# Kernel optimization log

Hardware: AMD Instinct MI355X
Metric: run time of the kernel (lower is better)

## Reference

```python
import jax, jax.numpy as jnp
import numpy as np

N, D, H, O, E, K = 4096, 512, 1024, 512, 8, 2


def setup_inputs() -> dict:
    key = jax.random.key(0)
    ks = jax.random.split(key, 7)
    s = 0.02
    return {
        "x": jax.random.normal(ks[0], (N, D), dtype=jnp.float32),
        "W1": jax.random.normal(ks[1], (E, D, H), dtype=jnp.float32) * s,
        "b1": jnp.zeros((E, H), dtype=jnp.float32),
        "W2": jax.random.normal(ks[2], (E, H, O), dtype=jnp.float32) * s,
        "b2": jnp.zeros((E, O), dtype=jnp.float32),
        "Wg": jax.random.normal(ks[3], (D, E), dtype=jnp.float32) * s,
        "bg": jnp.zeros((E,), dtype=jnp.float32),
        "k": K,
    }


def reference(x, W1, b1, W2, b2, Wg, bg, k):
    # Gating: softmax over experts, then top-k with renormalized weights
    gates = jax.nn.softmax(x @ Wg + bg, axis=1)              # [N, E]
    topv, topi = jax.lax.top_k(gates, k)                     # [N, k]
    w = topv / jnp.sum(topv, axis=1, keepdims=True)          # renormalized top-k weights

    # Dense per-expert two-layer MLP (grouped GEMM form)
    h = jax.nn.relu(jnp.einsum('nd,edh->neh', x, W1) + b1[None])   # [N, E, H]
    y = jnp.einsum('neh,eho->neo', h, W2) + b2[None]               # [N, E, O]

    # Gather selected experts and combine
    y_sel = jnp.take_along_axis(y, topi[:, :, None], axis=1)       # [N, k, O]
    out = jnp.einsum('nko,nk->no', y_sel, w)                       # [N, O]
    return out, gates, topi
```

## Files before the change

kernel.cpp:

```cpp
#include <hip/hip_runtime.h>
#include <hip/hip_bf16.h>

#define N_TOK 4096
#define DIM   512
#define HID   1024
#define OUTD  512
#define NEXP  8
#define TOPK  2

#define MT1 72
#define HROWS 9216

typedef __bf16 bf16;
typedef bf16  bf16x8 __attribute__((ext_vector_type(8)));
typedef bf16  bf16x4 __attribute__((ext_vector_type(4)));
typedef float f32x4  __attribute__((ext_vector_type(4)));

__device__ inline f32x4 mfma16(bf16x8 a, bf16x8 b, f32x4 c) {
    return __builtin_amdgcn_mfma_f32_16x16x32_bf16(a, b, c, 0, 0, 0);
}

__device__ inline void gload16(const bf16* g, char* l) {
    __builtin_amdgcn_global_load_lds(
        (const __attribute__((address_space(1))) void*)g,
        (__attribute__((address_space(3))) void*)l, 16, 0, 0);
}

__global__ __launch_bounds__(256) void prep_kernel(
    const float* __restrict__ W1, const float* __restrict__ W2,
    const float* __restrict__ Wg,
    bf16* __restrict__ W1t, bf16* __restrict__ W2t, float* __restrict__ WgT)
{
    int b = blockIdx.x;
    if (b == 8192) {
        for (int i = threadIdx.x; i < DIM * NEXP; i += 256) {
            int d = i >> 3, e = i & 7;
            WgT[e * DIM + d] = Wg[i];
        }
        return;
    }
    const float* src; bf16* dst; int R, C, tilex, rem, e;
    if (b < 4096) {
        e = b >> 9; rem = b & 511; R = DIM; C = HID; tilex = 32;
        src = W1; dst = W1t;
    } else {
        b -= 4096;
        e = b >> 9; rem = b & 511; R = HID; C = OUTD; tilex = 16;
        src = W2; dst = W2t;
    }
    const float* s = src + (size_t)e * R * C;
    bf16* d = dst + (size_t)e * R * C;
    int c0 = (rem % tilex) * 32, r0 = (rem / tilex) * 32;

    __shared__ float tile[32][33];
    int tx = threadIdx.x & 31, ty = threadIdx.x >> 5;
#pragma unroll
    for (int i = 0; i < 4; ++i) {
        int r = ty + i * 8;
        tile[r][tx] = s[(size_t)(r0 + r) * C + c0 + tx];
    }
    __syncthreads();
#pragma unroll
    for (int i = 0; i < 4; ++i) {
        int r = ty + i * 8;
        d[(size_t)(c0 + r) * R + r0 + tx] = (bf16)tile[tx][r];
    }
}

__global__ __launch_bounds__(256) void gate_kernel(
    const float* __restrict__ x, const float* __restrict__ WgT,
    const float* __restrict__ bg, bf16* __restrict__ xb,
    float* __restrict__ gates_out, float* __restrict__ topi_out,
    int* __restrict__ pick_e, float* __restrict__ pick_w)
{
    int wave = threadIdx.x >> 6;
    int lane = threadIdx.x & 63;
    int n = blockIdx.x * 4 + wave;

    const float4* x4 = (const float4*)(x + (size_t)n * DIM);
    float4 v0 = x4[lane];
    float4 v1 = x4[lane + 64];

    bf16x4 o0 = { (bf16)v0.x, (bf16)v0.y, (bf16)v0.z, (bf16)v0.w };
    bf16x4 o1 = { (bf16)v1.x, (bf16)v1.y, (bf16)v1.z, (bf16)v1.w };
    bf16x4* xb4 = (bf16x4*)(xb + (size_t)n * DIM);
    xb4[lane]      = o0;
    xb4[lane + 64] = o1;

    float acc[NEXP];
#pragma unroll
    for (int e = 0; e < NEXP; ++e) {
        const float4* wr = (const float4*)(WgT + e * DIM);
        float4 w0 = wr[lane];
        float4 w1 = wr[lane + 64];
        acc[e] = v0.x * w0.x + v0.y * w0.y + v0.z * w0.z + v0.w * w0.w
               + v1.x * w1.x + v1.y * w1.y + v1.z * w1.z + v1.w * w1.w;
    }
#pragma unroll
    for (int off = 32; off >= 1; off >>= 1) {
#pragma unroll
        for (int e = 0; e < NEXP; ++e) acc[e] += __shfl_xor(acc[e], off, 64);
    }
#pragma unroll
    for (int e = 0; e < NEXP; ++e) acc[e] += bg[e];

    float m = acc[0];
#pragma unroll
    for (int e = 1; e < NEXP; ++e) m = fmaxf(m, acc[e]);
    float g[NEXP];
    float s = 0.f;
#pragma unroll
    for (int e = 0; e < NEXP; ++e) { g[e] = expf(acc[e] - m); s += g[e]; }
    float inv_s = 1.f / s;
#pragma unroll
    for (int e = 0; e < NEXP; ++e) g[e] *= inv_s;

    if (lane < NEXP) gates_out[n * NEXP + lane] = g[lane];

    if (lane == 0) {
        int m1 = 0;
#pragma unroll
        for (int e = 1; e < NEXP; ++e) if (g[e] > g[m1]) m1 = e;
        int m2 = (m1 == 0) ? 1 : 0;
#pragma unroll
        for (int e = 0; e < NEXP; ++e) if (e != m1 && g[e] > g[m2]) m2 = e;
        float v1g = g[m1], v2g = g[m2];
        float inv = 1.f / (v1g + v2g);
        topi_out[n * TOPK + 0] = (float)m1;
        topi_out[n * TOPK + 1] = (float)m2;
        int2 pe = { m1, m2 };
        float2 pw = { v1g * inv, v2g * inv };
        *(int2*)(pick_e + n * 2) = pe;
        *(float2*)(pick_w + n * 2) = pw;
    }
}

__global__ __launch_bounds__(256) void bucket_kernel(
    const int* __restrict__ pick_e,
    int* __restrict__ counts, int* __restrict__ tlist)
{
    __shared__ int cnt;
    if (threadIdx.x == 0) cnt = 0;
    __syncthreads();
    int e = blockIdx.x;
    for (int i = threadIdx.x; i < N_TOK * 2; i += 256) {
        if (pick_e[i] == e) {
            int p = atomicAdd(&cnt, 1);
            tlist[e * N_TOK + p] = i;
        }
    }
    __syncthreads();
    if (threadIdx.x == 0) counts[e] = cnt;
}

__global__ void sched_kernel(const int* __restrict__ counts, int* __restrict__ meta)
{
    if (threadIdx.x != 0) return;
    int* hdr = meta;
    int* s1 = meta + 2;
    int base = 0, t1 = 0;
    for (int e = 0; e < NEXP; ++e) {
        int c = counts[e];
        int n1 = (c + 127) >> 7;
        for (int lt = 0; lt < n1; ++lt) {
            s1[t1 * 3] = e; s1[t1 * 3 + 1] = base + lt * 128; s1[t1 * 3 + 2] = lt * 128; ++t1;
        }
        base += n1 << 7;
    }
    hdr[0] = t1;
}

__global__ __launch_bounds__(256, 2) void l1_kernel(
    const bf16* __restrict__ xb, const bf16* __restrict__ W1t,
    const float* __restrict__ b1, const int* __restrict__ counts,
    const int* __restrict__ tlist, const int* __restrict__ meta,
    bf16* __restrict__ h)
{
    int mt = blockIdx.x >> 3, nt = blockIdx.x & 7;
    if (mt >= meta[0]) return;
    const int* s1 = meta + 2 + mt * 3;
    int e = s1[0], rb = s1[1], i0 = s1[2];
    int cnt = counts[e];

    __shared__ __align__(16) char lds[32768];

    int tid = threadIdx.x, w = tid >> 6, l = tid & 63;
    int c0 = w * 128 + l, c1 = c0 + 64;
    int rA0 = c0 >> 2, kA0 = c0 & 3;
    int rA1 = c1 >> 2, kA1 = c1 & 3;
    int iA0 = i0 + rA0, iA1 = i0 + rA1;
    int tok0 = iA0 < cnt ? (tlist[e * N_TOK + iA0] >> 1) : 0;
    int tok1 = iA1 < cnt ? (tlist[e * N_TOK + iA1] >> 1) : 0;
    const bf16* sA0 = xb + (size_t)tok0 * DIM + kA0 * 8;
    const bf16* sA1 = xb + (size_t)tok1 * DIM + kA1 * 8;
    int n0 = nt * 128;
    const bf16* w1e = W1t + (size_t)e * HID * DIM;
    const bf16* sB0 = w1e + (size_t)(n0 + rA0) * DIM + kA0 * 8;
    const bf16* sB1 = w1e + (size_t)(n0 + rA1) * DIM + kA1 * 8;
    int oA0 = c0 * 16, oA1 = c1 * 16;

    f32x4 acc[4][4];
#pragma unroll
    for (int mf = 0; mf < 4; ++mf)
#pragma unroll
        for (int nf = 0; nf < 4; ++nf) acc[mf][nf] = (f32x4){0.f, 0.f, 0.f, 0.f};

    int wm = w >> 1, wn = w & 1;
    int lr = l & 15, kb = (l >> 4) * 16;

    {
        char* A = lds;       char* B = lds + 8192;
        gload16(sA0, A + oA0); gload16(sA1, A + oA1);
        gload16(sB0, B + oA0); gload16(sB1, B + oA1);
    }

    for (int ks = 0; ks < 16; ++ks) {
        __syncthreads();
        if (ks < 15) {
            char* A = lds + (((ks + 1) & 1) * 16384);
            char* B = A + 8192;
            int kof = (ks + 1) * 32;
            gload16(sA0 + kof, A + oA0); gload16(sA1 + kof, A + oA1);
            gload16(sB0 + kof, B + oA0); gload16(sB1 + kof, B + oA1);
        }
        char* A = lds + ((ks & 1) * 16384);
        char* B = A + 8192;
        bf16x8 af[4], bfr[4];
#pragma unroll
        for (int mf = 0; mf < 4; ++mf)
            af[mf] = *(const bf16x8*)(A + (wm * 64 + mf * 16 + lr) * 64 + kb);
#pragma unroll
        for (int nf = 0; nf < 4; ++nf)
            bfr[nf] = *(const bf16x8*)(B + (wn * 64 + nf * 16 + lr) * 64 + kb);
#pragma unroll
        for (int mf = 0; mf < 4; ++mf)
#pragma unroll
            for (int nf = 0; nf < 4; ++nf)
                acc[mf][nf] = mfma16(af[mf], bfr[nf], acc[mf][nf]);
    }

    const float* b1e = b1 + e * HID;
#pragma unroll
    for (int nf = 0; nf < 4; ++nf) {
        int colg = n0 + wn * 64 + nf * 16 + lr;
        float bias = b1e[colg];
#pragma unroll
        for (int mf = 0; mf < 4; ++mf) {
#pragma unroll
            for (int r = 0; r < 4; ++r) {
                int gr = rb + wm * 64 + mf * 16 + (l >> 4) * 4 + r;
                float v = fmaxf(acc[mf][nf][r] + bias, 0.f);
                h[(size_t)gr * HID + colg] = (bf16)v;
            }
        }
    }
}

__global__ __launch_bounds__(256, 2) void l2_kernel(
    const bf16* __restrict__ h, const bf16* __restrict__ W2t,
    const int* __restrict__ counts, const int* __restrict__ tlist,
    const int* __restrict__ meta, bf16* __restrict__ ybuf)
{
    int mt = blockIdx.x >> 2, nt = blockIdx.x & 3;
    if (mt >= meta[0]) return;
    const int* s1 = meta + 2 + mt * 3;
    int e = s1[0], rb = s1[1], i0 = s1[2];
    int cnt = counts[e];

    __shared__ __align__(16) char lds[32768];

    int tid = threadIdx.x, w = tid >> 6, l = tid & 63;
    int c0 = w * 128 + l, c1 = c0 + 64;
    int rA0 = c0 >> 2, kA0 = c0 & 3;
    int rA1 = c1 >> 2, kA1 = c1 & 3;
    const bf16* sA0 = h + (size_t)(rb + rA0) * HID + kA0 * 8;
    const bf16* sA1 = h + (size_t)(rb + rA1) * HID + kA1 * 8;
    int n0 = nt * 128;
    const bf16* w2e = W2t + (size_t)e * OUTD * HID;
    const bf16* sB0 = w2e + (size_t)(n0 + rA0) * HID + kA0 * 8;
    const bf16* sB1 = w2e + (size_t)(n0 + rA1) * HID + kA1 * 8;
    int oA0 = c0 * 16, oA1 = c1 * 16;

    f32x4 acc[4][4];
#pragma unroll
    for (int mf = 0; mf < 4; ++mf)
#pragma unroll
        for (int nf = 0; nf < 4; ++nf) acc[mf][nf] = (f32x4){0.f, 0.f, 0.f, 0.f};

    int wm = w >> 1, wn = w & 1;
    int lr = l & 15, kb = (l >> 4) * 16;

    {
        char* A = lds;       char* B = lds + 8192;
        gload16(sA0, A + oA0); gload16(sA1, A + oA1);
        gload16(sB0, B + oA0); gload16(sB1, B + oA1);
    }

    for (int ks = 0; ks < 32; ++ks) {
        __syncthreads();
        if (ks < 31) {
            char* A = lds + (((ks + 1) & 1) * 16384);
            char* B = A + 8192;
            int kof = (ks + 1) * 32;
            gload16(sA0 + kof, A + oA0); gload16(sA1 + kof, A + oA1);
            gload16(sB0 + kof, B + oA0); gload16(sB1 + kof, B + oA1);
        }
        char* A = lds + ((ks & 1) * 16384);
        char* B = A + 8192;
        bf16x8 af[4], bfr[4];
#pragma unroll
        for (int mf = 0; mf < 4; ++mf)
            af[mf] = *(const bf16x8*)(A + (wm * 64 + mf * 16 + lr) * 64 + kb);
#pragma unroll
        for (int nf = 0; nf < 4; ++nf)
            bfr[nf] = *(const bf16x8*)(B + (wn * 64 + nf * 16 + lr) * 64 + kb);
#pragma unroll
        for (int mf = 0; mf < 4; ++mf)
#pragma unroll
            for (int nf = 0; nf < 4; ++nf)
                acc[mf][nf] = mfma16(af[mf], bfr[nf], acc[mf][nf]);
    }

#pragma unroll
    for (int mf = 0; mf < 4; ++mf) {
#pragma unroll
        for (int r = 0; r < 4; ++r) {
            int rloc = wm * 64 + mf * 16 + (l >> 4) * 4 + r;
            int i = i0 + rloc;
            if (i < cnt) {
                int pi = tlist[e * N_TOK + i];
                bf16* yrow = ybuf + (size_t)pi * OUTD;
#pragma unroll
                for (int nf = 0; nf < 4; ++nf) {
                    int colg = n0 + wn * 64 + nf * 16 + lr;
                    yrow[colg] = (bf16)acc[mf][nf][r];
                }
            }
        }
    }
}

__global__ __launch_bounds__(256) void combine_kernel(
    const bf16* __restrict__ ybuf, const float* __restrict__ b2,
    const int* __restrict__ pick_e, const float* __restrict__ pick_w,
    float* __restrict__ out)
{
    int wave = threadIdx.x >> 6;
    int lane = threadIdx.x & 63;
    int n = blockIdx.x * 4 + wave;

    int e0 = pick_e[n * 2], e1 = pick_e[n * 2 + 1];
    float w0 = pick_w[n * 2], w1 = pick_w[n * 2 + 1];

    const bf16x8* y0 = (const bf16x8*)(ybuf + (size_t)(n * 2) * OUTD);
    const bf16x8* y1 = (const bf16x8*)(ybuf + (size_t)(n * 2 + 1) * OUTD);
    const float4* b20 = (const float4*)(b2 + e0 * OUTD);
    const float4* b21 = (const float4*)(b2 + e1 * OUTD);
    float4* o4 = (float4*)(out + (size_t)n * OUTD);

    bf16x8 a = y0[lane];
    bf16x8 b = y1[lane];
    float4 c0 = b20[lane * 2], c1 = b20[lane * 2 + 1];
    float4 d0 = b21[lane * 2], d1 = b21[lane * 2 + 1];

    float4 r0, r1;
    r0.x = w0 * ((float)a[0] + c0.x) + w1 * ((float)b[0] + d0.x);
    r0.y = w0 * ((float)a[1] + c0.y) + w1 * ((float)b[1] + d0.y);
    r0.z = w0 * ((float)a[2] + c0.z) + w1 * ((float)b[2] + d0.z);
    r0.w = w0 * ((float)a[3] + c0.w) + w1 * ((float)b[3] + d0.w);
    r1.x = w0 * ((float)a[4] + c1.x) + w1 * ((float)b[4] + d1.x);
    r1.y = w0 * ((float)a[5] + c1.y) + w1 * ((float)b[5] + d1.y);
    r1.z = w0 * ((float)a[6] + c1.z) + w1 * ((float)b[6] + d1.z);
    r1.w = w0 * ((float)a[7] + c1.w) + w1 * ((float)b[7] + d1.w);
    o4[lane * 2]     = r0;
    o4[lane * 2 + 1] = r1;
}

extern "C" void kernel_launch(void* const* d_in, const int* in_sizes, int n_in,
                              void* d_out, int out_size, void* d_ws, size_t ws_size,
                              hipStream_t stream)
{
    const float* x  = (const float*)d_in[0];
    const float* W1 = (const float*)d_in[1];
    const float* b1 = (const float*)d_in[2];
    const float* W2 = (const float*)d_in[3];
    const float* b2 = (const float*)d_in[4];
    const float* Wg = (const float*)d_in[5];
    const float* bg = (const float*)d_in[6];

    float* out_f   = (float*)d_out;
    float* gates_o = out_f + (size_t)N_TOK * OUTD;
    float* topi_o  = gates_o + (size_t)N_TOK * NEXP;

    char* ws = (char*)d_ws;
    size_t offW1t  = 0;
    size_t offW2t  = offW1t + (size_t)NEXP * HID * DIM * 2;
    size_t offXb   = offW2t + (size_t)NEXP * OUTD * HID * 2;
    size_t offH    = offXb + (size_t)N_TOK * DIM * 2;
    size_t offYb   = offH + (size_t)HROWS * HID * 2;
    size_t offCnt  = offYb + (size_t)N_TOK * 2 * OUTD * 2;
    size_t offTl   = offCnt + 256;
    size_t offMeta = offTl + (size_t)NEXP * N_TOK * 4;
    size_t offPkE  = offMeta + 4096;
    size_t offPkW  = offPkE + (size_t)N_TOK * 2 * 4;
    size_t offWgT  = offPkW + (size_t)N_TOK * 2 * 4;

    bf16*  W1t    = (bf16*)(ws + offW1t);
    bf16*  W2t    = (bf16*)(ws + offW2t);
    bf16*  xbuf   = (bf16*)(ws + offXb);
    bf16*  hbuf   = (bf16*)(ws + offH);
    bf16*  ybuf   = (bf16*)(ws + offYb);
    int*   cnts   = (int*)(ws + offCnt);
    int*   tlist  = (int*)(ws + offTl);
    int*   meta   = (int*)(ws + offMeta);
    int*   pick_e = (int*)(ws + offPkE);
    float* pick_w = (float*)(ws + offPkW);
    float* WgT    = (float*)(ws + offWgT);

    prep_kernel<<<8193, 256, 0, stream>>>(W1, W2, Wg, W1t, W2t, WgT);

    gate_kernel<<<N_TOK / 4, 256, 0, stream>>>(x, WgT, bg, xbuf, gates_o, topi_o,
                                               pick_e, pick_w);

    bucket_kernel<<<NEXP, 256, 0, stream>>>(pick_e, cnts, tlist);

    sched_kernel<<<1, 64, 0, stream>>>(cnts, meta);

    l1_kernel<<<MT1 * 8, 256, 0, stream>>>(xbuf, W1t, b1, cnts, tlist, meta, hbuf);
    l2_kernel<<<MT1 * 4, 256, 0, stream>>>(hbuf, W2t, cnts, tlist, meta, ybuf);

    combine_kernel<<<N_TOK / 4, 256, 0, stream>>>(ybuf, b2, pick_e, pick_w, out_f);
}
```

Before: 87.71 us.

## Fuse prep with gating, merge bucket and schedule, swizzle LDS, raise occupancy

Merges weight transposition and gating into one launch, with each gating block transposing Wg into shared memory instead of reading a global WgT. Bucketing and schedule building become a single one-block kernel using per-expert shared atomics. The GEMM kernels XOR-swizzle the LDS k-chunk placement to reduce bank conflicts and raise launch bounds to 4 blocks per CU. The transpose store is vectorised to 4-element bf16 writes. Each gating block now redoes the Wg transpose, and the higher occupancy target may cause register spills.

```diff
diff --git a/kernel.cpp b/kernel.cpp
--- a/kernel.cpp
+++ b/kernel.cpp
@@ -26,19 +26,94 @@
         (__attribute__((address_space(3))) void*)l, 16, 0, 0);
 }
 
-__global__ __launch_bounds__(256) void prep_kernel(
+__global__ __launch_bounds__(256) void prep_gate_kernel(
     const float* __restrict__ W1, const float* __restrict__ W2,
-    const float* __restrict__ Wg,
-    bf16* __restrict__ W1t, bf16* __restrict__ W2t, float* __restrict__ WgT)
-{
+    const float* __restrict__ Wg, const float* __restrict__ bg,
+    const float* __restrict__ x,
+    bf16* __restrict__ W1t, bf16* __restrict__ W2t,
+    bf16* __restrict__ xb,
+    float* __restrict__ gates_out, float* __restrict__ topi_out,
+    int* __restrict__ pick_e, float* __restrict__ pick_w)
+{
+    __shared__ __align__(16) float smem[NEXP * DIM];
     int b = blockIdx.x;
-    if (b == 8192) {
-        for (int i = threadIdx.x; i < DIM * NEXP; i += 256) {
-            int d = i >> 3, e = i & 7;
-            WgT[e * DIM + d] = Wg[i];
+
+    if (b >= 8192) {
+        const float4* Wg4 = (const float4*)Wg;
+        for (int i = threadIdx.x; i < DIM * NEXP / 4; i += 256) {
+            float4 v = Wg4[i];
+#pragma unroll
+            for (int j = 0; j < 4; ++j) {
+                int idx = i * 4 + j;
+                smem[(idx & 7) * DIM + (idx >> 3)] = ((const float*)&v)[j];
+            }
+        }
+        __syncthreads();
+
+        int wave = threadIdx.x >> 6;
+        int lane = threadIdx.x & 63;
+        int n = (b - 8192) * 4 + wave;
+
+        const float4* x4 = (const float4*)(x + (size_t)n * DIM);
+        float4 v0 = x4[lane];
+        float4 v1 = x4[lane + 64];
+
+        bf16x4 o0 = { (bf16)v0.x, (bf16)v0.y, (bf16)v0.z, (bf16)v0.w };
+        bf16x4 o1 = { (bf16)v1.x, (bf16)v1.y, (bf16)v1.z, (bf16)v1.w };
+        bf16x4* xb4 = (bf16x4*)(xb + (size_t)n * DIM);
+        xb4[lane]      = o0;
+        xb4[lane + 64] = o1;
+
+        float acc[NEXP];
+#pragma unroll
+        for (int e = 0; e < NEXP; ++e) {
+            const float4* wr = (const float4*)(smem + e * DIM);
+            float4 w0 = wr[lane];
+            float4 w1 = wr[lane + 64];
+            acc[e] = v0.x * w0.x + v0.y * w0.y + v0.z * w0.z + v0.w * w0.w
+                   + v1.x * w1.x + v1.y * w1.y + v1.z * w1.z + v1.w * w1.w;
+        }
+#pragma unroll
+        for (int off = 32; off >= 1; off >>= 1) {
+#pragma unroll
+            for (int e = 0; e < NEXP; ++e) acc[e] += __shfl_xor(acc[e], off, 64);
+        }
+#pragma unroll
+        for (int e = 0; e < NEXP; ++e) acc[e] += bg[e];
+
+        float m = acc[0];
+#pragma unroll
+        for (int e = 1; e < NEXP; ++e) m = fmaxf(m, acc[e]);
+        float g[NEXP];
+        float s = 0.f;
+#pragma unroll
+        for (int e = 0; e < NEXP; ++e) { g[e] = expf(acc[e] - m); s += g[e]; }
+        float inv_s = 1.f / s;
+#pragma unroll
+        for (int e = 0; e < NEXP; ++e) g[e] *= inv_s;
+
+        if (lane < NEXP) gates_out[n * NEXP + lane] = g[lane];
+
+        if (lane == 0) {
+            int m1 = 0;
+#pragma unroll
+            for (int e = 1; e < NEXP; ++e) if (g[e] > g[m1]) m1 = e;
+            int m2 = (m1 == 0) ? 1 : 0;
+#pragma unroll
+            for (int e = 0; e < NEXP; ++e) if (e != m1 && g[e] > g[m2]) m2 = e;
+            float v1g = g[m1], v2g = g[m2];
+            float inv = 1.f / (v1g + v2g);
+            topi_out[n * TOPK + 0] = (float)m1;
+            topi_out[n * TOPK + 1] = (float)m2;
+            int2 pe = { m1, m2 };
+            float2 pw = { v1g * inv, v2g * inv };
+            *(int2*)(pick_e + n * 2) = pe;
+            *(float2*)(pick_w + n * 2) = pw;
         }
         return;
     }
+
+    float (*tile)[33] = (float(*)[33])smem;
     const float* src; bf16* dst; int R, C, tilex, rem, e;
     if (b < 4096) {
         e = b >> 9; rem = b & 511; R = DIM; C = HID; tilex = 32;
@@ -52,7 +127,6 @@
     bf16* d = dst + (size_t)e * R * C;
     int c0 = (rem % tilex) * 32, r0 = (rem / tilex) * 32;
 
-    __shared__ float tile[32][33];
     int tx = threadIdx.x & 31, ty = threadIdx.x >> 5;
 #pragma unroll
     for (int i = 0; i < 4; ++i) {
@@ -60,117 +134,48 @@
         tile[r][tx] = s[(size_t)(r0 + r) * C + c0 + tx];
     }
     __syncthreads();
-#pragma unroll
-    for (int i = 0; i < 4; ++i) {
-        int r = ty + i * 8;
-        d[(size_t)(c0 + r) * R + r0 + tx] = (bf16)tile[tx][r];
-    }
-}
-
-__global__ __launch_bounds__(256) void gate_kernel(
-    const float* __restrict__ x, const float* __restrict__ WgT,
-    const float* __restrict__ bg, bf16* __restrict__ xb,
-    float* __restrict__ gates_out, float* __restrict__ topi_out,
-    int* __restrict__ pick_e, float* __restrict__ pick_w)
-{
-    int wave = threadIdx.x >> 6;
-    int lane = threadIdx.x & 63;
-    int n = blockIdx.x * 4 + wave;
-
-    const float4* x4 = (const float4*)(x + (size_t)n * DIM);
-    float4 v0 = x4[lane];
-    float4 v1 = x4[lane + 64];
-
-    bf16x4 o0 = { (bf16)v0.x, (bf16)v0.y, (bf16)v0.z, (bf16)v0.w };
-    bf16x4 o1 = { (bf16)v1.x, (bf16)v1.y, (bf16)v1.z, (bf16)v1.w };
-    bf16x4* xb4 = (bf16x4*)(xb + (size_t)n * DIM);
-    xb4[lane]      = o0;
-    xb4[lane + 64] = o1;
-
-    float acc[NEXP];
-#pragma unroll
-    for (int e = 0; e < NEXP; ++e) {
-        const float4* wr = (const float4*)(WgT + e * DIM);
-        float4 w0 = wr[lane];
-        float4 w1 = wr[lane + 64];
-        acc[e] = v0.x * w0.x + v0.y * w0.y + v0.z * w0.z + v0.w * w0.w
-               + v1.x * w1.x + v1.y * w1.y + v1.z * w1.z + v1.w * w1.w;
-    }
-#pragma unroll
-    for (int off = 32; off >= 1; off >>= 1) {
-#pragma unroll
-        for (int e = 0; e < NEXP; ++e) acc[e] += __shfl_xor(acc[e], off, 64);
-    }
-#pragma unroll
-    for (int e = 0; e < NEXP; ++e) acc[e] += bg[e];
-
-    float m = acc[0];
-#pragma unroll
-    for (int e = 1; e < NEXP; ++e) m = fmaxf(m, acc[e]);
-    float g[NEXP];
-    float s = 0.f;
-#pragma unroll
-    for (int e = 0; e < NEXP; ++e) { g[e] = expf(acc[e] - m); s += g[e]; }
-    float inv_s = 1.f / s;
-#pragma unroll
-    for (int e = 0; e < NEXP; ++e) g[e] *= inv_s;
-
-    if (lane < NEXP) gates_out[n * NEXP + lane] = g[lane];
-
-    if (lane == 0) {
-        int m1 = 0;
-#pragma unroll
-        for (int e = 1; e < NEXP; ++e) if (g[e] > g[m1]) m1 = e;
-        int m2 = (m1 == 0) ? 1 : 0;
-#pragma unroll
-        for (int e = 0; e < NEXP; ++e) if (e != m1 && g[e] > g[m2]) m2 = e;
-        float v1g = g[m1], v2g = g[m2];
-        float inv = 1.f / (v1g + v2g);
-        topi_out[n * TOPK + 0] = (float)m1;
-        topi_out[n * TOPK + 1] = (float)m2;
-        int2 pe = { m1, m2 };
-        float2 pw = { v1g * inv, v2g * inv };
-        *(int2*)(pick_e + n * 2) = pe;
-        *(float2*)(pick_w + n * 2) = pw;
-    }
-}
-
-__global__ __launch_bounds__(256) void bucket_kernel(
+
+    int t = threadIdx.x;
+    int dc = t >> 3, q = t & 7;
+    bf16x4 v;
+#pragma unroll
+    for (int j = 0; j < 4; ++j) v[j] = (bf16)tile[q * 4 + j][dc];
+    *(bf16x4*)(d + (size_t)(c0 + dc) * R + r0 + q * 4) = v;
+}
+
+__global__ __launch_bounds__(1024) void bucket_sched_kernel(
     const int* __restrict__ pick_e,
-    int* __restrict__ counts, int* __restrict__ tlist)
-{
-    __shared__ int cnt;
-    if (threadIdx.x == 0) cnt = 0;
+    int* __restrict__ counts, int* __restrict__ tlist, int* __restrict__ meta)
+{
+    __shared__ int cnt[NEXP];
+    if (threadIdx.x < NEXP) cnt[threadIdx.x] = 0;
     __syncthreads();
-    int e = blockIdx.x;
-    for (int i = threadIdx.x; i < N_TOK * 2; i += 256) {
-        if (pick_e[i] == e) {
-            int p = atomicAdd(&cnt, 1);
-            tlist[e * N_TOK + p] = i;
-        }
+    for (int i = threadIdx.x; i < N_TOK * 2; i += 1024) {
+        int e = pick_e[i];
+        int p = atomicAdd(&cnt[e], 1);
+        tlist[e * N_TOK + p] = i;
     }
     __syncthreads();
-    if (threadIdx.x == 0) counts[e] = cnt;
-}
-
-__global__ void sched_kernel(const int* __restrict__ counts, int* __restrict__ meta)
-{
-    if (threadIdx.x != 0) return;
-    int* hdr = meta;
-    int* s1 = meta + 2;
-    int base = 0, t1 = 0;
-    for (int e = 0; e < NEXP; ++e) {
-        int c = counts[e];
-        int n1 = (c + 127) >> 7;
-        for (int lt = 0; lt < n1; ++lt) {
-            s1[t1 * 3] = e; s1[t1 * 3 + 1] = base + lt * 128; s1[t1 * 3 + 2] = lt * 128; ++t1;
-        }
-        base += n1 << 7;
-    }
-    hdr[0] = t1;
-}
-
-__global__ __launch_bounds__(256, 2) void l1_kernel(
+    if (threadIdx.x == 0) {
+        int base = 0, t1 = 0;
+        for (int e = 0; e < NEXP; ++e) {
+            int c = cnt[e];
+            counts[e] = c;
+            int n1 = (c + 127) >> 7;
+            for (int lt = 0; lt < n1; ++lt) {
+                meta[2 + t1 * 3]     = e;
+                meta[2 + t1 * 3 + 1] = base + lt * 128;
+                meta[2 + t1 * 3 + 2] = lt * 128;
+                ++t1;
+            }
+            base += n1 << 7;
+        }
+        meta[0] = t1;
+    }
+}
+
+
+__global__ __launch_bounds__(256, 4) void l1_kernel(
     const bf16* __restrict__ xb, const bf16* __restrict__ W1t,
     const float* __restrict__ b1, const int* __restrict__ counts,
     const int* __restrict__ tlist, const int* __restrict__ meta,
@@ -186,8 +191,9 @@
 
     int tid = threadIdx.x, w = tid >> 6, l = tid & 63;
     int c0 = w * 128 + l, c1 = c0 + 64;
-    int rA0 = c0 >> 2, kA0 = c0 & 3;
-    int rA1 = c1 >> 2, kA1 = c1 & 3;
+    int rA0 = c0 >> 2, rA1 = c1 >> 2;
+    int kA0 = (c0 & 3) ^ ((rA0 & 3) ^ ((rA0 >> 2) & 1));
+    int kA1 = (c1 & 3) ^ ((rA1 & 3) ^ ((rA1 >> 2) & 1));
     int iA0 = i0 + rA0, iA1 = i0 + rA1;
     int tok0 = iA0 < cnt ? (tlist[e * N_TOK + iA0] >> 1) : 0;
     int tok1 = iA1 < cnt ? (tlist[e * N_TOK + iA1] >> 1) : 0;
@@ -206,7 +212,8 @@
         for (int nf = 0; nf < 4; ++nf) acc[mf][nf] = (f32x4){0.f, 0.f, 0.f, 0.f};
 
     int wm = w >> 1, wn = w & 1;
-    int lr = l & 15, kb = (l >> 4) * 16;
+    int lr = l & 15;
+    int kb = (((l >> 4) ^ ((l & 3) ^ ((l >> 2) & 1)))) * 16;
 
     {
         char* A = lds;       char* B = lds + 8192;
@@ -256,7 +263,7 @@
     }
 }
 
-__global__ __launch_bounds__(256, 2) void l2_kernel(
+__global__ __launch_bounds__(256, 4) void l2_kernel(
     const bf16* __restrict__ h, const bf16* __restrict__ W2t,
     const int* __restrict__ counts, const int* __restrict__ tlist,
     const int* __restrict__ meta, bf16* __restrict__ ybuf)
@@ -271,8 +278,9 @@
 
     int tid = threadIdx.x, w = tid >> 6, l = tid & 63;
     int c0 = w * 128 + l, c1 = c0 + 64;
-    int rA0 = c0 >> 2, kA0 = c0 & 3;
-    int rA1 = c1 >> 2, kA1 = c1 & 3;
+    int rA0 = c0 >> 2, rA1 = c1 >> 2;
+    int kA0 = (c0 & 3) ^ ((rA0 & 3) ^ ((rA0 >> 2) & 1));
+    int kA1 = (c1 & 3) ^ ((rA1 & 3) ^ ((rA1 >> 2) & 1));
     const bf16* sA0 = h + (size_t)(rb + rA0) * HID + kA0 * 8;
     const bf16* sA1 = h + (size_t)(rb + rA1) * HID + kA1 * 8;
     int n0 = nt * 128;
@@ -288,7 +296,8 @@
         for (int nf = 0; nf < 4; ++nf) acc[mf][nf] = (f32x4){0.f, 0.f, 0.f, 0.f};
 
     int wm = w >> 1, wn = w & 1;
-    int lr = l & 15, kb = (l >> 4) * 16;
+    int lr = l & 15;
+    int kb = (((l >> 4) ^ ((l & 3) ^ ((l >> 2) & 1)))) * 16;
 
     {
         char* A = lds;       char* B = lds + 8192;
@@ -403,7 +412,6 @@
     size_t offMeta = offTl + (size_t)NEXP * N_TOK * 4;
     size_t offPkE  = offMeta + 4096;
     size_t offPkW  = offPkE + (size_t)N_TOK * 2 * 4;
-    size_t offWgT  = offPkW + (size_t)N_TOK * 2 * 4;
 
     bf16*  W1t    = (bf16*)(ws + offW1t);
     bf16*  W2t    = (bf16*)(ws + offW2t);
@@ -415,16 +423,11 @@
     int*   meta   = (int*)(ws + offMeta);
     int*   pick_e = (int*)(ws + offPkE);
     float* pick_w = (float*)(ws + offPkW);
-    float* WgT    = (float*)(ws + offWgT);
-
-    prep_kernel<<<8193, 256, 0, stream>>>(W1, W2, Wg, W1t, W2t, WgT);
-
-    gate_kernel<<<N_TOK / 4, 256, 0, stream>>>(x, WgT, bg, xbuf, gates_o, topi_o,
-                                               pick_e, pick_w);
-
-    bucket_kernel<<<NEXP, 256, 0, stream>>>(pick_e, cnts, tlist);
-
-    sched_kernel<<<1, 64, 0, stream>>>(cnts, meta);
+
+    prep_gate_kernel<<<8192 + N_TOK / 4, 256, 0, stream>>>(
+        W1, W2, Wg, bg, x, W1t, W2t, xbuf, gates_o, topi_o, pick_e, pick_w);
+
+    bucket_sched_kernel<<<1, 1024, 0, stream>>>(pick_e, cnts, tlist, meta);
 
     l1_kernel<<<MT1 * 8, 256, 0, stream>>>(xbuf, W1t, b1, cnts, tlist, meta, hbuf);
     l2_kernel<<<MT1 * 4, 256, 0, stream>>>(hbuf, W2t, cnts, tlist, meta, ybuf);
```

Result: faster. 76.94 us (-12.3%).
